# Kernel tuning notes

Measured on AMD Instinct MI355X. Metric: run time of the kernel, lower is better.

Reference implementation:

```python
import jax, jax.numpy as jnp
import numpy as np

B, T, D, H = 2, 2048, 1024, 16
NEG = -65504.0


def setup_inputs() -> dict:
    key = jax.random.key(0)
    ks = jax.random.split(key, 12)
    std = float(np.sqrt(2.0 / (D + D)))  # xavier_normal for square weights
    inp = {
        'q': jax.random.normal(ks[0], (B, T, D), jnp.float32),
        'k': jax.random.normal(ks[1], (B, T, D), jnp.float32),
        'v': jax.random.normal(ks[2], (B, T, D), jnp.float32),
        'mask': jax.random.randint(ks[3], (B, T), 0, 2, jnp.int32),
        # weights stored as (in, out) so y = x @ W + b
        'Wq': jax.random.normal(ks[4], (D, D), jnp.float32) * std,
        'bq': jnp.zeros((D,), jnp.float32),
        'Wk': jax.random.normal(ks[5], (D, D), jnp.float32) * std,
        'bk': jnp.zeros((D,), jnp.float32),
        'Wv': jax.random.normal(ks[6], (D, D), jnp.float32) * std,
        'bv': jnp.zeros((D,), jnp.float32),
        'Wo': jax.random.normal(ks[7], (D, D), jnp.float32) * std,
        'bo': jnp.zeros((D,), jnp.float32),
    }
    return inp


def reference(q, k, v, mask, Wq, bq, Wk, bk, Wv, bv, Wo, bo):
    b, t, _ = q.shape
    dim_a = Wq.shape[1]
    dh = dim_a // H
    # projections, then split into heads: (b, t, H, dh)
    qh = (q @ Wq + bq).reshape(b, t, H, dh)
    kh = (k @ Wk + bk).reshape(b, t, H, dh)
    vh = (v @ Wv + bv).reshape(b, t, H, dh)
    # NOTE: module scales by 1/sqrt(dim_a) with the FULL dim_a, not per-head
    a = jnp.einsum('bthd,bshd->bhts', qh, kh) / jnp.sqrt(jnp.float32(dim_a))
    # 2D mask broadcasts over query positions: (b, 1, 1, t_keys)
    a = jnp.where(mask[:, None, None, :] == 0, NEG, a)
    a = jax.nn.softmax(a, axis=-1)  # dropout_prob=0 (eval mode)
    o = jnp.einsum('bhts,bshd->bthd', a, vh).reshape(b, t, dim_a)
    return o @ Wo + bo
```

## Files before the change

kernel.cpp:

```cpp
#include <hip/hip_runtime.h>
#include <hip/hip_bf16.h>
#include <math.h>

#define B_ 2
#define T_ 2048
#define D_ 1024
#define H_ 16
#define QSCALE (0.03125f * 1.44269504088896f)

typedef _Float16 f16;
using f16x4 = __attribute__((ext_vector_type(4))) _Float16;
using f16x8 = __attribute__((ext_vector_type(8))) _Float16;
using f32x4 = __attribute__((ext_vector_type(4))) float;

__device__ __forceinline__ void gl16(const void* g, void* l) {
  __builtin_amdgcn_global_load_lds(
      (__attribute__((address_space(1))) void*)g,
      (__attribute__((address_space(3))) void*)l, 16, 0, 0);
}

__global__ __launch_bounds__(256) void prep(
    const float* __restrict__ q, const float* __restrict__ k,
    const float* __restrict__ v, const int* __restrict__ mask,
    const float* __restrict__ Wq, const float* __restrict__ Wk,
    const float* __restrict__ Wv, const float* __restrict__ Wo,
    const float* __restrict__ bq, const float* __restrict__ bk,
    const float* __restrict__ bv, const float* __restrict__ bo,
    f16* __restrict__ xqkv, f16* __restrict__ Wt, float* __restrict__ bias,
    int* __restrict__ idx, int* __restrict__ nk) {
  __shared__ float sh[64][65];
  const int bid = blockIdx.x;
  const int tid = threadIdx.x;

  if (bid < 6144) {
    const int z = bid / 2048;
    const float* src = (z == 0) ? q : (z == 1) ? k : v;
    const size_t i = ((size_t)(bid % 2048) * 256 + tid) * 8;
    float4 a = *(const float4*)(src + i);
    float4 b = *(const float4*)(src + i + 4);
    f16x8 o;
    o[0] = (f16)a.x; o[1] = (f16)a.y; o[2] = (f16)a.z; o[3] = (f16)a.w;
    o[4] = (f16)b.x; o[5] = (f16)b.y; o[6] = (f16)b.z; o[7] = (f16)b.w;
    *(f16x8*)(xqkv + (size_t)z * 4194304 + i) = o;
  } else if (bid < 7168) {
    const int id = bid - 6144;
    const int z = id >> 8;
    const int k0 = ((id >> 4) & 15) * 64, n0 = (id & 15) * 64;
    const float* W = (z == 0) ? Wq : (z == 1) ? Wk : (z == 2) ? Wv : Wo;
    const int r = tid >> 2, c0 = (tid & 3) * 16;
#pragma unroll
    for (int i = 0; i < 4; ++i)
      *(float4*)&sh[r][c0 + 4 * i] =
          *(const float4*)&W[(size_t)(k0 + r) * 1024 + n0 + c0 + 4 * i];
    __syncthreads();
    f16 tmp[16];
#pragma unroll
    for (int i = 0; i < 16; ++i) tmp[i] = (f16)sh[c0 + i][r];
    f16* dst = Wt + (size_t)z * 1048576 + (size_t)(n0 + r) * 1024 + k0 + c0;
    *(f16x8*)dst = *(f16x8*)&tmp[0];
    *(f16x8*)(dst + 8) = *(f16x8*)&tmp[8];
  } else if (bid < 7184) {
    const int i = (bid - 7168) * 256 + tid;
    const int z = i >> 10;
    const float* s = (z == 0) ? bq : (z == 1) ? bk : (z == 2) ? bv : bo;
    bias[i] = s[i & 1023];
  } else {
    const int b = bid - 7184;
    int* cnt = (int*)sh;
    int loc[8];
    int c = 0;
#pragma unroll
    for (int i = 0; i < 8; ++i) {
      loc[i] = mask[b * T_ + tid * 8 + i];
      c += loc[i];
    }
    cnt[tid] = c;
    __syncthreads();
    for (int off = 1; off < 256; off <<= 1) {
      int vsh = (tid >= off) ? cnt[tid - off] : 0;
      __syncthreads();
      cnt[tid] += vsh;
      __syncthreads();
    }
    int pos = cnt[tid] - c;
#pragma unroll
    for (int i = 0; i < 8; ++i)
      if (loc[i]) idx[b * T_ + pos++] = tid * 8 + i;
    if (tid == 255) nk[b] = cnt[255];
  }
}

template <int TM, typename OT>
__global__ __launch_bounds__(256) void gemm_bt(
    const f16* __restrict__ Xb, const f16* __restrict__ Wtb,
    const float* __restrict__ biasb, OT* __restrict__ Cb,
    int M, int N, int K, float qscale) {
  constexpr int FM = TM / 32;
  __shared__ __align__(16) f16 As[TM * 32];
  __shared__ __align__(16) f16 Bs[128 * 32];
  const int z = blockIdx.z;
  const f16* X  = Xb  + (size_t)z * M * K;
  const f16* Wt = Wtb + (size_t)z * N * K;
  const float* bias = biasb + (size_t)z * N;
  OT* C = Cb + (size_t)z * M * N;
  const float scl = (z == 0) ? qscale : 1.f;

  const int tid = threadIdx.x;
  const int wave = tid >> 6, lane = tid & 63;
  const int quad = lane >> 4, l16 = lane & 15;
  const int wm = wave & 1, wn = wave >> 1;
  const int m0 = blockIdx.y * TM, n0 = blockIdx.x * 128;

  f32x4 acc[FM][4] = {};

  const f16* asrc = X  + (size_t)(m0 + (tid >> 2)) * K + (tid & 3) * 8;
  const f16* bsrc = Wt + (size_t)(n0 + (tid >> 2)) * K + (tid & 3) * 8;
  char* aldst = (char*)As + tid * 16;
  char* bldst = (char*)Bs + tid * 16;
  const size_t rstep = (size_t)64 * K;

  const int NK = K >> 5;
  for (int kt = 0; kt < NK; ++kt) {
    if (kt) __syncthreads();
    gl16(asrc, aldst);
    if constexpr (TM == 128) gl16(asrc + rstep, aldst + 4096);
    gl16(bsrc, bldst);
    gl16(bsrc + rstep, bldst + 4096);
    asrc += 32; bsrc += 32;
    __syncthreads();

    f16x8 af[FM], bf[4];
#pragma unroll
    for (int t = 0; t < FM; ++t)
      af[t] = *(const f16x8*)&As[((TM / 2) * wm + 16 * t + l16) * 32 + quad * 8];
#pragma unroll
    for (int t = 0; t < 4; ++t)
      bf[t] = *(const f16x8*)&Bs[(64 * wn + 16 * t + l16) * 32 + quad * 8];
#pragma unroll
    for (int i = 0; i < FM; ++i)
#pragma unroll
      for (int j = 0; j < 4; ++j)
        acc[i][j] = __builtin_amdgcn_mfma_f32_16x16x32_f16(af[i], bf[j], acc[i][j], 0, 0, 0);
  }

  const int cm = m0 + (TM / 2) * wm + 4 * quad;
  const int cn = n0 + 64 * wn + l16;
#pragma unroll
  for (int tn = 0; tn < 4; ++tn) {
    const float bv = bias[cn + 16 * tn];
#pragma unroll
    for (int tm = 0; tm < FM; ++tm)
#pragma unroll
      for (int r = 0; r < 4; ++r)
        C[(size_t)(cm + 16 * tm + r) * N + cn + 16 * tn] = (OT)((acc[tm][tn][r] + bv) * scl);
  }
}

__global__ __launch_bounds__(256) void kgather(
    const f16* __restrict__ kh, const int* __restrict__ idx,
    const int* __restrict__ nk, f16* __restrict__ khc) {
  const int b = blockIdx.y;
  const int n = nk[b];
  const int nkt = (n + 63) >> 6;
  if ((int)blockIdx.x >= nkt) return;
  const int j0 = blockIdx.x * 64;
  const int r2 = threadIdx.x >> 7;
  const int col = threadIdx.x & 127;
  for (int rr = 0; rr < 32; ++rr) {
    const int j = j0 + rr * 2 + r2;
    uint4 val = {0u, 0u, 0u, 0u};
    if (j < n) {
      const int t = idx[b * T_ + j];
      val = *(const uint4*)(kh + ((size_t)b * T_ + t) * D_ + col * 8);
    }
    *(uint4*)(khc + ((size_t)b * T_ + j) * D_ + col * 8) = val;
  }
}

__global__ __launch_bounds__(256) void vtrans(
    const f16* __restrict__ vh, const int* __restrict__ idx,
    const int* __restrict__ nk, f16* __restrict__ vhT) {
  const int tt = blockIdx.x, bh = blockIdx.y;
  const int b = bh >> 4, h = bh & 15;
  const int n = nk[b];
  const int nkt = (n + 63) >> 6;
  if (tt >= nkt) return;
  __shared__ f16 t[64][72];
  const int tid = threadIdx.x;
  const int r = tid >> 2, cq = 16 * (tid & 3);

  const int j = tt * 64 + r;
  uint4 v0 = {0u, 0u, 0u, 0u}, v1 = {0u, 0u, 0u, 0u};
  if (j < n) {
    const int tsrc = idx[b * T_ + j];
    const uint4* src = (const uint4*)(vh + ((size_t)b * T_ + tsrc) * D_ + h * 64 + cq);
    v0 = src[0]; v1 = src[1];
  }
  *(uint4*)&t[r][cq]     = v0;
  *(uint4*)&t[r][cq + 8] = v1;
  __syncthreads();

  f16 tmp[16];
#pragma unroll
  for (int xx = 0; xx < 16; ++xx) {
    int x = (xx + r) & 15;
    tmp[x] = t[cq + x][r];
  }
  f16* dst = vhT + ((size_t)bh * 64 + r) * T_ + tt * 64 + cq;
  *(uint4*)&dst[0] = *(uint4*)&tmp[0];
  *(uint4*)&dst[8] = *(uint4*)&tmp[8];
}

__global__ __launch_bounds__(256) void attn_mfma(
    const f16* __restrict__ qh, const f16* __restrict__ khc,
    const f16* __restrict__ vhT, const int* __restrict__ nkd,
    f16* __restrict__ oat) {
  __shared__ f16 Qs[64][72];
  __shared__ f16 Ks[64][72];
  __shared__ f16 Vt[64][72];
  __shared__ f16 Ps[4][16][72];

  const int qt = blockIdx.x, bh = blockIdx.y;
  const int b = bh >> 4, h = bh & 15;
  const int tid = threadIdx.x;
  const int wave = tid >> 6, lane = tid & 63;
  const int quad = lane >> 4, l16 = lane & 15;
  const int sr = tid >> 2, sq = 16 * (tid & 3);

  const int n = nkd[b];
  const int nkt = (n + 63) >> 6;
  const int npad = (nkt << 6) - n;

  {
    const uint4* src = (const uint4*)(qh + ((size_t)(b * T_ + qt * 64 + sr)) * D_ + h * 64 + sq);
    *(uint4*)&Qs[sr][sq]     = src[0];
    *(uint4*)&Qs[sr][sq + 8] = src[1];
  }
  __syncthreads();
  const f16x8 qf0 = *(const f16x8*)&Qs[wave * 16 + l16][quad * 8];
  const f16x8 qf1 = *(const f16x8*)&Qs[wave * 16 + l16][32 + quad * 8];

  float lsum = 0.f;
  f32x4 o[4] = {};

  const f16* kbase = khc + (size_t)b * T_ * D_ + h * 64;
  const f16* vbase = vhT + ((size_t)bh * 64 + sr) * T_;

  uint4 kr0, kr1, vr0, vr1;
  auto load_kv = [&](int kt) {
    const uint4* ks = (const uint4*)(kbase + (size_t)(kt * 64 + sr) * D_ + sq);
    kr0 = ks[0]; kr1 = ks[1];
    const uint4* vs = (const uint4*)(vbase + kt * 64 + sq);
    vr0 = vs[0]; vr1 = vs[1];
  };
  if (nkt > 0) load_kv(0);

  for (int kt = 0; kt < nkt; ++kt) {
    *(uint4*)&Ks[sr][sq]     = kr0;
    *(uint4*)&Ks[sr][sq + 8] = kr1;
    *(uint4*)&Vt[sr][sq]     = vr0;
    *(uint4*)&Vt[sr][sq + 8] = vr1;
    __syncthreads();
    if (kt + 1 < nkt) load_kv(kt + 1);

#pragma unroll
    for (int tn = 0; tn < 4; ++tn) {
      f16x8 kf0 = *(const f16x8*)&Ks[16 * tn + l16][quad * 8];
      f16x8 kf1 = *(const f16x8*)&Ks[16 * tn + l16][32 + quad * 8];
      f32x4 s = {0.f, 0.f, 0.f, 0.f};
      s = __builtin_amdgcn_mfma_f32_16x16x32_f16(kf0, qf0, s, 0, 0, 0);
      s = __builtin_amdgcn_mfma_f32_16x16x32_f16(kf1, qf1, s, 0, 0, 0);
      float p0 = exp2f(s[0]);
      float p1 = exp2f(s[1]);
      float p2 = exp2f(s[2]);
      float p3 = exp2f(s[3]);
      lsum += (p0 + p1) + (p2 + p3);
      f16x4 pk;
      pk[0] = (f16)p0; pk[1] = (f16)p1; pk[2] = (f16)p2; pk[3] = (f16)p3;
      *(f16x4*)&Ps[wave][l16][16 * tn + 4 * quad] = pk;
    }

    f16x8 pf0 = *(const f16x8*)&Ps[wave][l16][quad * 8];
    f16x8 pf1 = *(const f16x8*)&Ps[wave][l16][32 + quad * 8];
#pragma unroll
    for (int t = 0; t < 4; ++t) {
      f16x8 vf0 = *(const f16x8*)&Vt[16 * t + l16][quad * 8];
      f16x8 vf1 = *(const f16x8*)&Vt[16 * t + l16][32 + quad * 8];
      o[t] = __builtin_amdgcn_mfma_f32_16x16x32_f16(pf0, vf0, o[t], 0, 0, 0);
      o[t] = __builtin_amdgcn_mfma_f32_16x16x32_f16(pf1, vf1, o[t], 0, 0, 0);
    }
    __syncthreads();
  }

  lsum += __shfl_xor(lsum, 16);
  lsum += __shfl_xor(lsum, 32);
  lsum -= (float)npad;
  float inv[4];
#pragma unroll
  for (int r = 0; r < 4; ++r) inv[r] = 1.f / __shfl(lsum, 4 * quad + r);

  const size_t orow = (size_t)(b * T_ + qt * 64 + wave * 16 + 4 * quad);
#pragma unroll
  for (int r = 0; r < 4; ++r)
#pragma unroll
    for (int t = 0; t < 4; ++t)
      oat[(orow + r) * D_ + h * 64 + 16 * t + l16] = (f16)(o[t][r] * inv[r]);
}

extern "C" void kernel_launch(void* const* d_in, const int* in_sizes, int n_in,
                              void* d_out, int out_size, void* d_ws, size_t ws_size,
                              hipStream_t stream) {
  const float* q  = (const float*)d_in[0];
  const float* k  = (const float*)d_in[1];
  const float* v  = (const float*)d_in[2];
  const int* mask = (const int*)d_in[3];
  const float* Wq = (const float*)d_in[4];
  const float* bq = (const float*)d_in[5];
  const float* Wk = (const float*)d_in[6];
  const float* bk = (const float*)d_in[7];
  const float* Wv = (const float*)d_in[8];
  const float* bv = (const float*)d_in[9];
  const float* Wo = (const float*)d_in[10];
  const float* bo = (const float*)d_in[11];
  float* out = (float*)d_out;

  char* ws = (char*)d_ws;
  f16* xqkv  = (f16*)(ws);
  f16* Wt    = (f16*)(ws + 25165824);
  float* bsw = (float*)(ws + 33554432);
  f16* qkvh  = (f16*)(ws + 33570816);
  int* idx   = (int*)(ws + 58736640);
  int* nk    = (int*)(ws + 58753024);
  f16* vhT   = (f16*)(ws);
  f16* oat   = (f16*)(ws + 8388608);
  f16* khc   = (f16*)(ws + 16777216);

  const int M = B_ * T_;
  dim3 blk(256);

  prep<<<dim3(7186), blk, 0, stream>>>(q, k, v, mask, Wq, Wk, Wv, Wo,
                                       bq, bk, bv, bo, xqkv, Wt, bsw, idx, nk);

  gemm_bt<128, f16><<<dim3(8, 32, 3), blk, 0, stream>>>(
      xqkv, Wt, bsw, qkvh, M, D_, D_, QSCALE);

  f16* qh = qkvh;
  f16* kh = qkvh + 4194304;
  f16* vh = qkvh + 8388608;

  kgather<<<dim3(32, 2), blk, 0, stream>>>(kh, idx, nk, khc);
  vtrans<<<dim3(32, 32), blk, 0, stream>>>(vh, idx, nk, vhT);

  attn_mfma<<<dim3(32, 32), blk, 0, stream>>>(qh, khc, vhT, nk, oat);

  gemm_bt<64, float><<<dim3(8, 64, 1), blk, 0, stream>>>(
      oat, Wt + 3145728, bsw + 3072, out, M, D_, D_, 1.f);
}
```

Baseline: 247.9 us.

## Fuse key compaction into QKV GEMM epilogue and double query rows per attention block

Prep now builds an inverse index from token to compacted key slot and zero-fills the key padding rows. The K projection GEMM then scatters its rows straight into the compacted key buffer, which removes the separate gather kernel and one pass over the key tensor. The attention kernel now handles 128 query rows per block, two 16-row groups per wave, with Q fragments loaded directly from global memory. Each K/V tile staged in LDS is reused for twice as many queries, at the cost of more registers and half as many blocks.

```diff
diff --git a/kernel.cpp b/kernel.cpp
--- a/kernel.cpp
+++ b/kernel.cpp
@@ -27,7 +27,8 @@
     const float* __restrict__ bq, const float* __restrict__ bk,
     const float* __restrict__ bv, const float* __restrict__ bo,
     f16* __restrict__ xqkv, f16* __restrict__ Wt, float* __restrict__ bias,
-    int* __restrict__ idx, int* __restrict__ nk) {
+    int* __restrict__ idx, int* __restrict__ inv, int* __restrict__ nk,
+    f16* __restrict__ khc) {
   __shared__ float sh[64][65];
   const int bid = blockIdx.x;
   const int tid = threadIdx.x;
@@ -84,17 +85,33 @@
     }
     int pos = cnt[tid] - c;
 #pragma unroll
-    for (int i = 0; i < 8; ++i)
-      if (loc[i]) idx[b * T_ + pos++] = tid * 8 + i;
-    if (tid == 255) nk[b] = cnt[255];
+    for (int i = 0; i < 8; ++i) {
+      const int t = tid * 8 + i;
+      if (loc[i]) {
+        idx[b * T_ + pos] = t;
+        inv[b * T_ + t] = pos;
+        ++pos;
+      } else {
+        inv[b * T_ + t] = -1;
+      }
+    }
+    const int n = cnt[255];
+    if (tid == 255) nk[b] = n;
+    const int nkt = (n + 63) >> 6;
+    const int npadrows = (nkt << 6) - n;
+    uint4 z4 = {0u, 0u, 0u, 0u};
+    f16* base = khc + ((size_t)b * T_ + n) * D_;
+    for (int i = tid; i < npadrows * 128; i += 256)
+      *(uint4*)(base + (size_t)i * 8) = z4;
   }
 }
 
 template <int TM, typename OT>
 __global__ __launch_bounds__(256) void gemm_bt(
     const f16* __restrict__ Xb, const f16* __restrict__ Wtb,
-    const float* __restrict__ biasb, OT* __restrict__ Cb,
-    int M, int N, int K, float qscale) {
+    const float* __restrict__ biasb, void* __restrict__ C0,
+    void* __restrict__ C1, void* __restrict__ C2,
+    const int* __restrict__ inv, int M, int N, int K, float qscale) {
   constexpr int FM = TM / 32;
   __shared__ __align__(16) f16 As[TM * 32];
   __shared__ __align__(16) f16 Bs[128 * 32];
@@ -102,7 +119,7 @@
   const f16* X  = Xb  + (size_t)z * M * K;
   const f16* Wt = Wtb + (size_t)z * N * K;
   const float* bias = biasb + (size_t)z * N;
-  OT* C = Cb + (size_t)z * M * N;
+  OT* C = (OT*)((z == 0) ? C0 : (z == 1) ? C1 : C2);
   const float scl = (z == 0) ? qscale : 1.f;
 
   const int tid = threadIdx.x;
@@ -145,35 +162,36 @@
 
   const int cm = m0 + (TM / 2) * wm + 4 * quad;
   const int cn = n0 + 64 * wn + l16;
-#pragma unroll
-  for (int tn = 0; tn < 4; ++tn) {
-    const float bv = bias[cn + 16 * tn];
+  float bv[4];
+#pragma unroll
+  for (int tn = 0; tn < 4; ++tn) bv[tn] = bias[cn + 16 * tn];
+
+  if (inv != nullptr && z == 1) {
+    const int bb = m0 >> 11;
+#pragma unroll
+    for (int tm = 0; tm < FM; ++tm) {
+#pragma unroll
+      for (int r = 0; r < 4; ++r) {
+        const int m = cm + 16 * tm + r;
+        const int j = inv[m];
+        if (j >= 0) {
+          OT* row = C + ((size_t)(bb << 11) + j) * N;
+#pragma unroll
+          for (int tn = 0; tn < 4; ++tn)
+            row[cn + 16 * tn] = (OT)(acc[tm][tn][r] + bv[tn]);
+        }
+      }
+    }
+  } else {
 #pragma unroll
     for (int tm = 0; tm < FM; ++tm)
 #pragma unroll
-      for (int r = 0; r < 4; ++r)
-        C[(size_t)(cm + 16 * tm + r) * N + cn + 16 * tn] = (OT)((acc[tm][tn][r] + bv) * scl);
-  }
-}
-
-__global__ __launch_bounds__(256) void kgather(
-    const f16* __restrict__ kh, const int* __restrict__ idx,
-    const int* __restrict__ nk, f16* __restrict__ khc) {
-  const int b = blockIdx.y;
-  const int n = nk[b];
-  const int nkt = (n + 63) >> 6;
-  if ((int)blockIdx.x >= nkt) return;
-  const int j0 = blockIdx.x * 64;
-  const int r2 = threadIdx.x >> 7;
-  const int col = threadIdx.x & 127;
-  for (int rr = 0; rr < 32; ++rr) {
-    const int j = j0 + rr * 2 + r2;
-    uint4 val = {0u, 0u, 0u, 0u};
-    if (j < n) {
-      const int t = idx[b * T_ + j];
-      val = *(const uint4*)(kh + ((size_t)b * T_ + t) * D_ + col * 8);
-    }
-    *(uint4*)(khc + ((size_t)b * T_ + j) * D_ + col * 8) = val;
+      for (int r = 0; r < 4; ++r) {
+        OT* row = C + (size_t)(cm + 16 * tm + r) * N;
+#pragma unroll
+        for (int tn = 0; tn < 4; ++tn)
+          row[cn + 16 * tn] = (OT)((acc[tm][tn][r] + bv[tn]) * scl);
+      }
   }
 }
 
@@ -215,10 +233,9 @@
     const f16* __restrict__ qh, const f16* __restrict__ khc,
     const f16* __restrict__ vhT, const int* __restrict__ nkd,
     f16* __restrict__ oat) {
-  __shared__ f16 Qs[64][72];
   __shared__ f16 Ks[64][72];
   __shared__ f16 Vt[64][72];
-  __shared__ f16 Ps[4][16][72];
+  __shared__ f16 Ps[4][32][72];
 
   const int qt = blockIdx.x, bh = blockIdx.y;
   const int b = bh >> 4, h = bh & 15;
@@ -231,17 +248,16 @@
   const int nkt = (n + 63) >> 6;
   const int npad = (nkt << 6) - n;
 
-  {
-    const uint4* src = (const uint4*)(qh + ((size_t)(b * T_ + qt * 64 + sr)) * D_ + h * 64 + sq);
-    *(uint4*)&Qs[sr][sq]     = src[0];
-    *(uint4*)&Qs[sr][sq + 8] = src[1];
-  }
-  __syncthreads();
-  const f16x8 qf0 = *(const f16x8*)&Qs[wave * 16 + l16][quad * 8];
-  const f16x8 qf1 = *(const f16x8*)&Qs[wave * 16 + l16][32 + quad * 8];
-
-  float lsum = 0.f;
-  f32x4 o[4] = {};
+  f16x8 qf[2][2];
+#pragma unroll
+  for (int gq = 0; gq < 2; ++gq) {
+    const f16* qp = qh + ((size_t)(b * T_ + qt * 128 + wave * 32 + 16 * gq + l16)) * D_ + h * 64 + quad * 8;
+    qf[gq][0] = *(const f16x8*)qp;
+    qf[gq][1] = *(const f16x8*)(qp + 32);
+  }
+
+  float lsum[2] = {0.f, 0.f};
+  f32x4 o[2][4] = {};
 
   const f16* kbase = khc + (size_t)b * T_ * D_ + h * 64;
   const f16* vbase = vhT + ((size_t)bh * 64 + sr) * T_;
@@ -267,44 +283,54 @@
     for (int tn = 0; tn < 4; ++tn) {
       f16x8 kf0 = *(const f16x8*)&Ks[16 * tn + l16][quad * 8];
       f16x8 kf1 = *(const f16x8*)&Ks[16 * tn + l16][32 + quad * 8];
-      f32x4 s = {0.f, 0.f, 0.f, 0.f};
-      s = __builtin_amdgcn_mfma_f32_16x16x32_f16(kf0, qf0, s, 0, 0, 0);
-      s = __builtin_amdgcn_mfma_f32_16x16x32_f16(kf1, qf1, s, 0, 0, 0);
-      float p0 = exp2f(s[0]);
-      float p1 = exp2f(s[1]);
-      float p2 = exp2f(s[2]);
-      float p3 = exp2f(s[3]);
-      lsum += (p0 + p1) + (p2 + p3);
-      f16x4 pk;
-      pk[0] = (f16)p0; pk[1] = (f16)p1; pk[2] = (f16)p2; pk[3] = (f16)p3;
-      *(f16x4*)&Ps[wave][l16][16 * tn + 4 * quad] = pk;
-    }
-
-    f16x8 pf0 = *(const f16x8*)&Ps[wave][l16][quad * 8];
-    f16x8 pf1 = *(const f16x8*)&Ps[wave][l16][32 + quad * 8];
+#pragma unroll
+      for (int gq = 0; gq < 2; ++gq) {
+        f32x4 s = {0.f, 0.f, 0.f, 0.f};
+        s = __builtin_amdgcn_mfma_f32_16x16x32_f16(kf0, qf[gq][0], s, 0, 0, 0);
+        s = __builtin_amdgcn_mfma_f32_16x16x32_f16(kf1, qf[gq][1], s, 0, 0, 0);
+        float p0 = exp2f(s[0]), p1 = exp2f(s[1]);
+        float p2 = exp2f(s[2]), p3 = exp2f(s[3]);
+        lsum[gq] += (p0 + p1) + (p2 + p3);
+        f16x4 pk;
+        pk[0] = (f16)p0; pk[1] = (f16)p1; pk[2] = (f16)p2; pk[3] = (f16)p3;
+        *(f16x4*)&Ps[wave][16 * gq + l16][16 * tn + 4 * quad] = pk;
+      }
+    }
+
+    f16x8 pf[2][2];
+#pragma unroll
+    for (int gq = 0; gq < 2; ++gq) {
+      pf[gq][0] = *(const f16x8*)&Ps[wave][16 * gq + l16][quad * 8];
+      pf[gq][1] = *(const f16x8*)&Ps[wave][16 * gq + l16][32 + quad * 8];
+    }
 #pragma unroll
     for (int t = 0; t < 4; ++t) {
       f16x8 vf0 = *(const f16x8*)&Vt[16 * t + l16][quad * 8];
       f16x8 vf1 = *(const f16x8*)&Vt[16 * t + l16][32 + quad * 8];
-      o[t] = __builtin_amdgcn_mfma_f32_16x16x32_f16(pf0, vf0, o[t], 0, 0, 0);
-      o[t] = __builtin_amdgcn_mfma_f32_16x16x32_f16(pf1, vf1, o[t], 0, 0, 0);
-    }
-    __syncthreads();
-  }
-
-  lsum += __shfl_xor(lsum, 16);
-  lsum += __shfl_xor(lsum, 32);
-  lsum -= (float)npad;
-  float inv[4];
-#pragma unroll
-  for (int r = 0; r < 4; ++r) inv[r] = 1.f / __shfl(lsum, 4 * quad + r);
-
-  const size_t orow = (size_t)(b * T_ + qt * 64 + wave * 16 + 4 * quad);
-#pragma unroll
-  for (int r = 0; r < 4; ++r)
-#pragma unroll
-    for (int t = 0; t < 4; ++t)
-      oat[(orow + r) * D_ + h * 64 + 16 * t + l16] = (f16)(o[t][r] * inv[r]);
+#pragma unroll
+      for (int gq = 0; gq < 2; ++gq) {
+        o[gq][t] = __builtin_amdgcn_mfma_f32_16x16x32_f16(pf[gq][0], vf0, o[gq][t], 0, 0, 0);
+        o[gq][t] = __builtin_amdgcn_mfma_f32_16x16x32_f16(pf[gq][1], vf1, o[gq][t], 0, 0, 0);
+      }
+    }
+    __syncthreads();
+  }
+
+#pragma unroll
+  for (int gq = 0; gq < 2; ++gq) {
+    float ls = lsum[gq];
+    ls += __shfl_xor(ls, 16);
+    ls += __shfl_xor(ls, 32);
+    ls -= (float)npad;
+    const size_t orow = (size_t)(b * T_ + qt * 128 + wave * 32 + 16 * gq + 4 * quad);
+#pragma unroll
+    for (int r = 0; r < 4; ++r) {
+      const float iv = 1.f / __shfl(ls, 4 * quad + r);
+#pragma unroll
+      for (int t = 0; t < 4; ++t)
+        oat[(orow + r) * D_ + h * 64 + 16 * t + l16] = (f16)(o[gq][t][r] * iv);
+    }
+  }
 }
 
 extern "C" void kernel_launch(void* const* d_in, const int* in_sizes, int n_in,
@@ -327,32 +353,30 @@
   char* ws = (char*)d_ws;
   f16* xqkv  = (f16*)(ws);
   f16* Wt    = (f16*)(ws + 25165824);
-  float* bsw = (float*)(ws + 33554432);
-  f16* qkvh  = (f16*)(ws + 33570816);
+  f16* qh    = (f16*)(ws + 33554432);
+  f16* vh    = (f16*)(ws + 41943040);
+  f16* khc   = (f16*)(ws + 50331648);
+  float* bsw = (float*)(ws + 58720256);
   int* idx   = (int*)(ws + 58736640);
-  int* nk    = (int*)(ws + 58753024);
+  int* inv   = (int*)(ws + 58753024);
+  int* nk    = (int*)(ws + 58769408);
   f16* vhT   = (f16*)(ws);
   f16* oat   = (f16*)(ws + 8388608);
-  f16* khc   = (f16*)(ws + 16777216);
 
   const int M = B_ * T_;
   dim3 blk(256);
 
   prep<<<dim3(7186), blk, 0, stream>>>(q, k, v, mask, Wq, Wk, Wv, Wo,
-                                       bq, bk, bv, bo, xqkv, Wt, bsw, idx, nk);
+                                       bq, bk, bv, bo, xqkv, Wt, bsw,
+                                       idx, inv, nk, khc);
 
   gemm_bt<128, f16><<<dim3(8, 32, 3), blk, 0, stream>>>(
-      xqkv, Wt, bsw, qkvh, M, D_, D_, QSCALE);
-
-  f16* qh = qkvh;
-  f16* kh = qkvh + 4194304;
-  f16* vh = qkvh + 8388608;
-
-  kgather<<<dim3(32, 2), blk, 0, stream>>>(kh, idx, nk, khc);
+      xqkv, Wt, bsw, qh, khc, vh, inv, M, D_, D_, QSCALE);
+
   vtrans<<<dim3(32, 32), blk, 0, stream>>>(vh, idx, nk, vhT);
 
-  attn_mfma<<<dim3(32, 32), blk, 0, stream>>>(qh, khc, vhT, nk, oat);
+  attn_mfma<<<dim3(16, 32), blk, 0, stream>>>(qh, khc, vhT, nk, oat);
 
   gemm_bt<64, float><<<dim3(8, 64, 1), blk, 0, stream>>>(
-      oat, Wt + 3145728, bsw + 3072, out, M, D_, D_, 1.f);
-}
+      oat, Wt + 3145728, bsw + 3072, out, out, out, nullptr, M, D_, D_, 1.f);
+}
```

After: 228.0 us. -8.0%, faster.
